# Kernel optimization log

Measured on AMD Instinct MI355X. Metric: run time of the kernel, lower is better.

## Reference

```python
import jax, jax.numpy as jnp
import numpy as np

B, T, E = 2, 2048, 1024
H = 16
D = E // H  # 64

def setup_inputs() -> dict:
    key = jax.random.key(0)
    kx, kq, kk, kv, ko = jax.random.split(key, 5)
    s = 1.0 / np.sqrt(E)
    return {
        "x":  jax.random.normal(kx, (B, T, E), dtype=jnp.float32),
        "Wq": jax.random.normal(kq, (E, E), dtype=jnp.float32) * s,
        "Wk": jax.random.normal(kk, (E, E), dtype=jnp.float32) * s,
        "Wv": jax.random.normal(kv, (E, E), dtype=jnp.float32) * s,
        "Wo": jax.random.normal(ko, (E, E), dtype=jnp.float32) * s,
    }

def reference(x, Wq, Wk, Wv, Wo):
    # Faithful to the torch module, including its quirks:
    #  - head split is a raw .view(B, H, T, D) reshape (NOT a transpose split)
    #  - masked_fill result is discarded in the original, so NO causal mask is applied
    #  - dropout = 0.0 -> identity
    b, t, e = x.shape
    q = jnp.reshape(x @ Wq, (b, H, t, D))
    k = jnp.reshape(x @ Wk, (b, H, t, D))
    v = jnp.reshape(x @ Wv, (b, H, t, D))
    # raw_score = q @ k^T ; softmax over keys of raw_score / sqrt(head_dim)
    scores = jnp.einsum("bhtd,bhsd->bhts", q, k) / jnp.sqrt(jnp.asarray(D, x.dtype))
    attn = jax.nn.softmax(scores, axis=-1)
    h = jnp.einsum("bhts,bhsd->bhtd", attn, v)           # (B,H,T,D)
    h = jnp.reshape(h, (b, t, e))                         # .view(B, T, -1)
    return h @ Wo
```

## Files before the change

### kernel.cpp

```cpp
#include <hip/hip_runtime.h>
#include <hip/hip_bf16.h>
#include <math.h>

#define BB 2
#define TT 2048
#define EE 1024
#define HH 16
#define DD 64
#define MM (BB*TT)

typedef __bf16 bf16;
typedef bf16 bf16x8 __attribute__((ext_vector_type(8)));
typedef bf16 bf16x4 __attribute__((ext_vector_type(4)));
typedef float f32x4 __attribute__((ext_vector_type(4)));

#define MFMA16(a,b,c) __builtin_amdgcn_mfma_f32_16x16x32_bf16((a),(b),(c),0,0,0)

__device__ __forceinline__ void gload_lds16(const void* g, void* l) {
  __builtin_amdgcn_global_load_lds(
      (const __attribute__((address_space(1))) unsigned int*)g,
      (__attribute__((address_space(3))) unsigned int*)l, 16, 0, 0);
}

__device__ __forceinline__ unsigned short bits(bf16 h) {
  return __builtin_bit_cast(unsigned short, h);
}

__global__ __launch_bounds__(256) void prep(const float* __restrict__ x,
                                            const float* __restrict__ w0,
                                            const float* __restrict__ w1,
                                            const float* __restrict__ w2,
                                            const float* __restrict__ w3,
                                            bf16* __restrict__ xb,
                                            bf16* t0, bf16* t1, bf16* t2, bf16* t3) {
  __shared__ bf16 tile[64][65];
  const int bid = blockIdx.x;
  if (bid < 4096) {
    const int i = bid * 256 + threadIdx.x;
    float4 f = ((const float4*)x)[i];
    bf16x4 h;
    h[0] = (bf16)f.x; h[1] = (bf16)f.y; h[2] = (bf16)f.z; h[3] = (bf16)f.w;
    ((bf16x4*)xb)[i] = h;
    return;
  }
  const int t = bid - 4096;
  const int z = t >> 8, rem = t & 255;
  const float* W = z == 0 ? w0 : z == 1 ? w1 : z == 2 ? w2 : w3;
  bf16* T = z == 0 ? t0 : z == 1 ? t1 : z == 2 ? t2 : t3;
  const int n0 = (rem & 15) * 64, k0 = (rem >> 4) * 64;
#pragma unroll
  for (int i = 0; i < 16; i++) {
    int idx = threadIdx.x + i * 256;
    int r = idx >> 6, c = idx & 63;
    tile[c][r] = (bf16)W[(size_t)(k0 + r) * EE + n0 + c];
  }
  __syncthreads();
#pragma unroll
  for (int i = 0; i < 16; i++) {
    int idx = threadIdx.x + i * 256;
    int r = idx >> 6, c = idx & 63;
    T[(size_t)(n0 + r) * EE + k0 + c] = tile[r][c];
  }
}

template <typename OutT>
__device__ __forceinline__ void gemm_core(const bf16* __restrict__ A, const bf16* __restrict__ Bt,
                                          OutT* __restrict__ C, bf16* As, bf16* Bs) {
  const int tid = threadIdx.x;
  const int w = tid >> 6, lane = tid & 63;
  const int lg = lane >> 4, lr = lane & 15;
  const int row0 = blockIdx.y * 128, col0 = blockIdx.x * 128;
  const int wrow = (w >> 1) * 64, wcol = (w & 1) * 64;
  f32x4 acc[4][4];
#pragma unroll
  for (int m = 0; m < 4; m++)
#pragma unroll
    for (int n = 0; n < 4; n++) acc[m][n] = f32x4{0.f, 0.f, 0.f, 0.f};

  for (int kt = 0; kt < EE; kt += 32) {
#pragma unroll
    for (int i = 0; i < 2; i++) {
      const int c = i * 4 + w;
      const int row = c * 16 + (lane >> 2);
      const int kof = (lane & 3) * 8;
      gload_lds16(A + (size_t)(row0 + row) * EE + kt + kof, &As[c * 512]);
      gload_lds16(Bt + (size_t)(col0 + row) * EE + kt + kof, &Bs[c * 512]);
    }
    __syncthreads();
    bf16x8 a[4], b[4];
#pragma unroll
    for (int m = 0; m < 4; m++)
      a[m] = *(const bf16x8*)&As[(wrow + m * 16 + lr) * 32 + lg * 8];
#pragma unroll
    for (int n = 0; n < 4; n++)
      b[n] = *(const bf16x8*)&Bs[(wcol + n * 16 + lr) * 32 + lg * 8];
#pragma unroll
    for (int m = 0; m < 4; m++)
#pragma unroll
      for (int n = 0; n < 4; n++) acc[m][n] = MFMA16(a[m], b[n], acc[m][n]);
    __syncthreads();
  }
#pragma unroll
  for (int m = 0; m < 4; m++)
#pragma unroll
    for (int n = 0; n < 4; n++)
#pragma unroll
      for (int r = 0; r < 4; r++) {
        const int rr = row0 + wrow + m * 16 + lg * 4 + r;
        const int cc = col0 + wcol + n * 16 + lr;
        C[(size_t)rr * EE + cc] = (OutT)acc[m][n][r];
      }
}

__global__ __launch_bounds__(256) void gemm_qkv(const bf16* __restrict__ A,
                                                const bf16* __restrict__ w0,
                                                const bf16* __restrict__ w1,
                                                const bf16* __restrict__ w2,
                                                bf16* o0, bf16* o1, bf16* o2) {
  __shared__ __align__(16) bf16 As[128 * 32];
  __shared__ __align__(16) bf16 Bs[128 * 32];
  const bf16* Bt = (blockIdx.z == 0) ? w0 : (blockIdx.z == 1) ? w1 : w2;
  bf16* C = (blockIdx.z == 0) ? o0 : (blockIdx.z == 1) ? o1 : o2;
  gemm_core<bf16>(A, Bt, C, As, Bs);
}

__global__ __launch_bounds__(256) void gemm_out(const bf16* __restrict__ A,
                                                const bf16* __restrict__ Bt,
                                                float* __restrict__ C) {
  __shared__ __align__(16) bf16 As[128 * 32];
  __shared__ __align__(16) bf16 Bs[128 * 32];
  gemm_core<float>(A, Bt, C, As, Bs);
}

__global__ __launch_bounds__(256, 2) void flash_attn(const bf16* __restrict__ Q,
                                                     const bf16* __restrict__ K,
                                                     const bf16* __restrict__ V,
                                                     bf16* __restrict__ Hout) {
  const int tid = threadIdx.x;
  const int w = tid >> 6, lane = tid & 63;
  const int hi = lane >> 4, lr = lane & 15;

  const int bid = blockIdx.x + 16 * blockIdx.y;
  const int sid = (bid & 7) * 64 + (bid >> 3);
  const int qb = sid & 15, bh = sid >> 4;

  const size_t base = (size_t)(bh >> 4) * TT * EE + (size_t)(bh & 15) * 128 * EE;
  const bf16* qh = Q + base;
  const bf16* kh = K + base;
  const bf16* vh = V + base;
  bf16* hh = Hout + base;
  const int r0w = qb * 128 + w * 32;

  __shared__ __align__(16) bf16 Ks[2][64 * 72];
  __shared__ __align__(16) bf16 Vt[2][64 * 72];
  __shared__ __align__(16) bf16 Ps[4 * 32 * 72];
  bf16* Pw = &Ps[w * 32 * 72];

  const float qscale = 0.18033688011112042f;
  bf16x8 aq[2][2];
#pragma unroll
  for (int rg = 0; rg < 2; rg++)
#pragma unroll
    for (int kk = 0; kk < 2; kk++) {
      bf16x8 qv = *(const bf16x8*)(qh + (size_t)(r0w + rg * 16 + lr) * DD + kk * 32 + hi * 8);
#pragma unroll
      for (int j = 0; j < 8; j++) qv[j] = (bf16)(qscale * (float)qv[j]);
      aq[rg][kk] = qv;
    }

  float l_[2] = {0.f, 0.f};
  f32x4 o[2][4];
#pragma unroll
  for (int rg = 0; rg < 2; rg++)
#pragma unroll
    for (int d = 0; d < 4; d++) o[rg][d] = f32x4{0.f, 0.f, 0.f, 0.f};

  const int krow = tid >> 2, kg8 = (tid & 3) * 8;
  const int vsp = tid & 31, vdb = (tid >> 5) * 4;

  bf16x8 kr0 = *(const bf16x8*)(kh + (size_t)krow * DD + kg8);
  bf16x8 kr1 = *(const bf16x8*)(kh + (size_t)krow * DD + kg8 + 32);
  bf16x4 va0 = *(const bf16x4*)(vh + (size_t)(2 * vsp) * DD + vdb);
  bf16x4 vb0 = *(const bf16x4*)(vh + (size_t)(2 * vsp + 1) * DD + vdb);
  bf16x4 va1 = *(const bf16x4*)(vh + (size_t)(2 * vsp) * DD + vdb + 32);
  bf16x4 vb1 = *(const bf16x4*)(vh + (size_t)(2 * vsp + 1) * DD + vdb + 32);
  *(bf16x8*)&Ks[0][krow * 72 + kg8] = kr0;
  *(bf16x8*)&Ks[0][krow * 72 + kg8 + 32] = kr1;
#pragma unroll
  for (int j = 0; j < 4; j++) {
    unsigned u0 = (unsigned)bits(va0[j]) | ((unsigned)bits(vb0[j]) << 16);
    unsigned u1 = (unsigned)bits(va1[j]) | ((unsigned)bits(vb1[j]) << 16);
    *(unsigned*)&Vt[0][(vdb + j) * 72 + 2 * vsp] = u0;
    *(unsigned*)&Vt[0][(vdb + 32 + j) * 72 + 2 * vsp] = u1;
  }
  kr0 = *(const bf16x8*)(kh + (size_t)(64 + krow) * DD + kg8);
  kr1 = *(const bf16x8*)(kh + (size_t)(64 + krow) * DD + kg8 + 32);
  va0 = *(const bf16x4*)(vh + (size_t)(64 + 2 * vsp) * DD + vdb);
  vb0 = *(const bf16x4*)(vh + (size_t)(64 + 2 * vsp + 1) * DD + vdb);
  va1 = *(const bf16x4*)(vh + (size_t)(64 + 2 * vsp) * DD + vdb + 32);
  vb1 = *(const bf16x4*)(vh + (size_t)(64 + 2 * vsp + 1) * DD + vdb + 32);
  __syncthreads();

  for (int t = 0; t < TT / 64; t++) {
    const bf16* Kc = Ks[t & 1];
    const bf16* Vc = Vt[t & 1];

    f32x4 sA[2][4];
#pragma unroll
    for (int rg = 0; rg < 2; rg++)
#pragma unroll
      for (int cf = 0; cf < 4; cf++) sA[rg][cf] = f32x4{0.f, 0.f, 0.f, 0.f};
#pragma unroll
    for (int cf = 0; cf < 4; cf++)
#pragma unroll
      for (int kk = 0; kk < 2; kk++) {
        bf16x8 bk = *(const bf16x8*)&Kc[(cf * 16 + lr) * 72 + kk * 32 + hi * 8];
#pragma unroll
        for (int rg = 0; rg < 2; rg++) sA[rg][cf] = MFMA16(bk, aq[rg][kk], sA[rg][cf]);
      }

#pragma unroll
    for (int rg = 0; rg < 2; rg++)
#pragma unroll
      for (int cf = 0; cf < 4; cf++) {
        bf16x4 pb;
#pragma unroll
        for (int r = 0; r < 4; r++) {
          float p = __builtin_amdgcn_exp2f(sA[rg][cf][r]);
          l_[rg] += p;
          pb[r] = (bf16)p;
        }
        *(bf16x4*)&Pw[(rg * 16 + lr) * 72 + cf * 16 + 4 * hi] = pb;
      }
    asm volatile("s_waitcnt lgkmcnt(0)" ::: "memory");

#pragma unroll
    for (int kk = 0; kk < 2; kk++) {
      bf16x8 bp[2];
#pragma unroll
      for (int rg = 0; rg < 2; rg++)
        bp[rg] = *(const bf16x8*)&Pw[(rg * 16 + lr) * 72 + kk * 32 + hi * 8];
#pragma unroll
      for (int dblk = 0; dblk < 4; dblk++) {
        bf16x8 av = *(const bf16x8*)&Vc[(dblk * 16 + lr) * 72 + kk * 32 + hi * 8];
#pragma unroll
        for (int rg = 0; rg < 2; rg++)
          o[rg][dblk] = MFMA16(av, bp[rg], o[rg][dblk]);
      }
    }

    if (t < TT / 64 - 1) {
      bf16* Kn = Ks[(t + 1) & 1];
      bf16* Vn = Vt[(t + 1) & 1];
      *(bf16x8*)&Kn[krow * 72 + kg8] = kr0;
      *(bf16x8*)&Kn[krow * 72 + kg8 + 32] = kr1;
#pragma unroll
      for (int j = 0; j < 4; j++) {
        unsigned u0 = (unsigned)bits(va0[j]) | ((unsigned)bits(vb0[j]) << 16);
        unsigned u1 = (unsigned)bits(va1[j]) | ((unsigned)bits(vb1[j]) << 16);
        *(unsigned*)&Vn[(vdb + j) * 72 + 2 * vsp] = u0;
        *(unsigned*)&Vn[(vdb + 32 + j) * 72 + 2 * vsp] = u1;
      }
      if (t < TT / 64 - 2) {
        const int s2 = (t + 2) * 64;
        kr0 = *(const bf16x8*)(kh + (size_t)(s2 + krow) * DD + kg8);
        kr1 = *(const bf16x8*)(kh + (size_t)(s2 + krow) * DD + kg8 + 32);
        va0 = *(const bf16x4*)(vh + (size_t)(s2 + 2 * vsp) * DD + vdb);
        vb0 = *(const bf16x4*)(vh + (size_t)(s2 + 2 * vsp + 1) * DD + vdb);
        va1 = *(const bf16x4*)(vh + (size_t)(s2 + 2 * vsp) * DD + vdb + 32);
        vb1 = *(const bf16x4*)(vh + (size_t)(s2 + 2 * vsp + 1) * DD + vdb + 32);
      }
    }
    __syncthreads();
  }

#pragma unroll
  for (int rg = 0; rg < 2; rg++) {
    float lt = l_[rg];
    lt += __shfl_xor(lt, 16);
    lt += __shfl_xor(lt, 32);
#pragma unroll
    for (int dblk = 0; dblk < 4; dblk++) {
      bf16x4 st;
#pragma unroll
      for (int r = 0; r < 4; r++) st[r] = (bf16)(o[rg][dblk][r] / lt);
      *(bf16x4*)(hh + (size_t)(r0w + rg * 16 + lr) * DD + dblk * 16 + 4 * hi) = st;
    }
  }
}

extern "C" void kernel_launch(void* const* d_in, const int* in_sizes, int n_in,
                              void* d_out, int out_size, void* d_ws, size_t ws_size,
                              hipStream_t stream) {
  const float* x  = (const float*)d_in[0];
  const float* Wq = (const float*)d_in[1];
  const float* Wk = (const float*)d_in[2];
  const float* Wv = (const float*)d_in[3];
  const float* Wo = (const float*)d_in[4];
  float* out = (float*)d_out;

  bf16* xb  = (bf16*)d_ws;
  bf16* wqt = xb + (size_t)MM * EE;
  bf16* wkt = wqt + (size_t)EE * EE;
  bf16* wvt = wkt + (size_t)EE * EE;
  bf16* wot = wvt + (size_t)EE * EE;
  bf16* Qb  = wot + (size_t)EE * EE;
  bf16* Kb  = Qb + (size_t)MM * EE;
  bf16* Vb  = Kb + (size_t)MM * EE;
  bf16* Hb  = xb;

  prep<<<dim3(5120), 256, 0, stream>>>(x, Wq, Wk, Wv, Wo, xb, wqt, wkt, wvt, wot);
  gemm_qkv<<<dim3(8, 32, 3), 256, 0, stream>>>(xb, wqt, wkt, wvt, Qb, Kb, Vb);
  flash_attn<<<dim3(16, 32), 256, 0, stream>>>(Qb, Kb, Vb, Hb);
  gemm_out<<<dim3(8, 32), 256, 0, stream>>>(Hb, wot, out);
}
```

Measured before the change: 122.3 us.

## Halve flash-attn query tile, load K fragments directly into registers

The attention kernel now gives each wave 16 query rows instead of 32, doubling the grid to 1024 blocks and raising the occupancy hint to 4 blocks per CU. K is no longer staged through LDS; each wave loads its MFMA K fragments straight from global memory into registers, prefetched one tile ahead. This cuts LDS traffic and footprint and improves parallelism. In exchange, K is reread from global/L2 by every wave, and reuse of each K/V tile across query rows is halved.

```diff
diff --git a/kernel.cpp b/kernel.cpp
--- a/kernel.cpp
+++ b/kernel.cpp
@@ -132,7 +132,7 @@
   gemm_core<float>(A, Bt, C, As, Bs);
 }
 
-__global__ __launch_bounds__(256, 2) void flash_attn(const bf16* __restrict__ Q,
+__global__ __launch_bounds__(256, 4) void flash_attn(const bf16* __restrict__ Q,
                                                      const bf16* __restrict__ K,
                                                      const bf16* __restrict__ V,
                                                      bf16* __restrict__ Hout) {
@@ -140,52 +140,49 @@
   const int w = tid >> 6, lane = tid & 63;
   const int hi = lane >> 4, lr = lane & 15;
 
-  const int bid = blockIdx.x + 16 * blockIdx.y;
-  const int sid = (bid & 7) * 64 + (bid >> 3);
-  const int qb = sid & 15, bh = sid >> 4;
+  const int bid = blockIdx.x + 32 * blockIdx.y;
+  const int sid = (bid & 7) * 128 + (bid >> 3);
+  const int qb = sid & 31, bh = sid >> 5;
 
   const size_t base = (size_t)(bh >> 4) * TT * EE + (size_t)(bh & 15) * 128 * EE;
   const bf16* qh = Q + base;
   const bf16* kh = K + base;
   const bf16* vh = V + base;
   bf16* hh = Hout + base;
-  const int r0w = qb * 128 + w * 32;
-
-  __shared__ __align__(16) bf16 Ks[2][64 * 72];
+  const int r0w = qb * 64 + w * 16;
+
   __shared__ __align__(16) bf16 Vt[2][64 * 72];
-  __shared__ __align__(16) bf16 Ps[4 * 32 * 72];
-  bf16* Pw = &Ps[w * 32 * 72];
+  __shared__ __align__(16) bf16 Ps[4 * 16 * 72];
+  bf16* Pw = &Ps[w * 16 * 72];
 
   const float qscale = 0.18033688011112042f;
-  bf16x8 aq[2][2];
-#pragma unroll
-  for (int rg = 0; rg < 2; rg++)
-#pragma unroll
-    for (int kk = 0; kk < 2; kk++) {
-      bf16x8 qv = *(const bf16x8*)(qh + (size_t)(r0w + rg * 16 + lr) * DD + kk * 32 + hi * 8);
-#pragma unroll
-      for (int j = 0; j < 8; j++) qv[j] = (bf16)(qscale * (float)qv[j]);
-      aq[rg][kk] = qv;
-    }
-
-  float l_[2] = {0.f, 0.f};
-  f32x4 o[2][4];
-#pragma unroll
-  for (int rg = 0; rg < 2; rg++)
-#pragma unroll
-    for (int d = 0; d < 4; d++) o[rg][d] = f32x4{0.f, 0.f, 0.f, 0.f};
-
-  const int krow = tid >> 2, kg8 = (tid & 3) * 8;
+  bf16x8 aq[2];
+#pragma unroll
+  for (int kk = 0; kk < 2; kk++) {
+    bf16x8 qv = *(const bf16x8*)(qh + (size_t)(r0w + lr) * DD + kk * 32 + hi * 8);
+#pragma unroll
+    for (int j = 0; j < 8; j++) qv[j] = (bf16)(qscale * (float)qv[j]);
+    aq[kk] = qv;
+  }
+
+  float l_ = 0.f;
+  f32x4 o[4];
+#pragma unroll
+  for (int d = 0; d < 4; d++) o[d] = f32x4{0.f, 0.f, 0.f, 0.f};
+
   const int vsp = tid & 31, vdb = (tid >> 5) * 4;
 
-  bf16x8 kr0 = *(const bf16x8*)(kh + (size_t)krow * DD + kg8);
-  bf16x8 kr1 = *(const bf16x8*)(kh + (size_t)krow * DD + kg8 + 32);
+  bf16x8 kf[4][2];
+#pragma unroll
+  for (int cf = 0; cf < 4; cf++)
+#pragma unroll
+    for (int kk = 0; kk < 2; kk++)
+      kf[cf][kk] = *(const bf16x8*)(kh + (size_t)(cf * 16 + lr) * DD + kk * 32 + hi * 8);
+
   bf16x4 va0 = *(const bf16x4*)(vh + (size_t)(2 * vsp) * DD + vdb);
   bf16x4 vb0 = *(const bf16x4*)(vh + (size_t)(2 * vsp + 1) * DD + vdb);
   bf16x4 va1 = *(const bf16x4*)(vh + (size_t)(2 * vsp) * DD + vdb + 32);
   bf16x4 vb1 = *(const bf16x4*)(vh + (size_t)(2 * vsp + 1) * DD + vdb + 32);
-  *(bf16x8*)&Ks[0][krow * 72 + kg8] = kr0;
-  *(bf16x8*)&Ks[0][krow * 72 + kg8 + 32] = kr1;
 #pragma unroll
   for (int j = 0; j < 4; j++) {
     unsigned u0 = (unsigned)bits(va0[j]) | ((unsigned)bits(vb0[j]) << 16);
@@ -193,8 +190,6 @@
     *(unsigned*)&Vt[0][(vdb + j) * 72 + 2 * vsp] = u0;
     *(unsigned*)&Vt[0][(vdb + 32 + j) * 72 + 2 * vsp] = u1;
   }
-  kr0 = *(const bf16x8*)(kh + (size_t)(64 + krow) * DD + kg8);
-  kr1 = *(const bf16x8*)(kh + (size_t)(64 + krow) * DD + kg8 + 32);
   va0 = *(const bf16x4*)(vh + (size_t)(64 + 2 * vsp) * DD + vdb);
   vb0 = *(const bf16x4*)(vh + (size_t)(64 + 2 * vsp + 1) * DD + vdb);
   va1 = *(const bf16x4*)(vh + (size_t)(64 + 2 * vsp) * DD + vdb + 32);
@@ -202,58 +197,50 @@
   __syncthreads();
 
   for (int t = 0; t < TT / 64; t++) {
-    const bf16* Kc = Ks[t & 1];
     const bf16* Vc = Vt[t & 1];
 
-    f32x4 sA[2][4];
-#pragma unroll
-    for (int rg = 0; rg < 2; rg++)
-#pragma unroll
-      for (int cf = 0; cf < 4; cf++) sA[rg][cf] = f32x4{0.f, 0.f, 0.f, 0.f};
+    f32x4 sA[4];
+#pragma unroll
+    for (int cf = 0; cf < 4; cf++) sA[cf] = f32x4{0.f, 0.f, 0.f, 0.f};
 #pragma unroll
     for (int cf = 0; cf < 4; cf++)
 #pragma unroll
-      for (int kk = 0; kk < 2; kk++) {
-        bf16x8 bk = *(const bf16x8*)&Kc[(cf * 16 + lr) * 72 + kk * 32 + hi * 8];
-#pragma unroll
-        for (int rg = 0; rg < 2; rg++) sA[rg][cf] = MFMA16(bk, aq[rg][kk], sA[rg][cf]);
-      }
-
-#pragma unroll
-    for (int rg = 0; rg < 2; rg++)
-#pragma unroll
-      for (int cf = 0; cf < 4; cf++) {
-        bf16x4 pb;
-#pragma unroll
-        for (int r = 0; r < 4; r++) {
-          float p = __builtin_amdgcn_exp2f(sA[rg][cf][r]);
-          l_[rg] += p;
-          pb[r] = (bf16)p;
-        }
-        *(bf16x4*)&Pw[(rg * 16 + lr) * 72 + cf * 16 + 4 * hi] = pb;
-      }
+      for (int kk = 0; kk < 2; kk++) sA[cf] = MFMA16(kf[cf][kk], aq[kk], sA[cf]);
+
+    if (t < TT / 64 - 1) {
+      const int s1 = (t + 1) * 64;
+#pragma unroll
+      for (int cf = 0; cf < 4; cf++)
+#pragma unroll
+        for (int kk = 0; kk < 2; kk++)
+          kf[cf][kk] = *(const bf16x8*)(kh + (size_t)(s1 + cf * 16 + lr) * DD + kk * 32 + hi * 8);
+    }
+
+#pragma unroll
+    for (int cf = 0; cf < 4; cf++) {
+      bf16x4 pb;
+#pragma unroll
+      for (int r = 0; r < 4; r++) {
+        float p = __builtin_amdgcn_exp2f(sA[cf][r]);
+        l_ += p;
+        pb[r] = (bf16)p;
+      }
+      *(bf16x4*)&Pw[lr * 72 + cf * 16 + 4 * hi] = pb;
+    }
     asm volatile("s_waitcnt lgkmcnt(0)" ::: "memory");
 
 #pragma unroll
     for (int kk = 0; kk < 2; kk++) {
-      bf16x8 bp[2];
-#pragma unroll
-      for (int rg = 0; rg < 2; rg++)
-        bp[rg] = *(const bf16x8*)&Pw[(rg * 16 + lr) * 72 + kk * 32 + hi * 8];
+      bf16x8 bp = *(const bf16x8*)&Pw[lr * 72 + kk * 32 + hi * 8];
 #pragma unroll
       for (int dblk = 0; dblk < 4; dblk++) {
         bf16x8 av = *(const bf16x8*)&Vc[(dblk * 16 + lr) * 72 + kk * 32 + hi * 8];
-#pragma unroll
-        for (int rg = 0; rg < 2; rg++)
-          o[rg][dblk] = MFMA16(av, bp[rg], o[rg][dblk]);
+        o[dblk] = MFMA16(av, bp, o[dblk]);
       }
     }
 
     if (t < TT / 64 - 1) {
-      bf16* Kn = Ks[(t + 1) & 1];
       bf16* Vn = Vt[(t + 1) & 1];
-      *(bf16x8*)&Kn[krow * 72 + kg8] = kr0;
-      *(bf16x8*)&Kn[krow * 72 + kg8 + 32] = kr1;
 #pragma unroll
       for (int j = 0; j < 4; j++) {
         unsigned u0 = (unsigned)bits(va0[j]) | ((unsigned)bits(vb0[j]) << 16);
@@ -263,8 +250,6 @@
       }
       if (t < TT / 64 - 2) {
         const int s2 = (t + 2) * 64;
-        kr0 = *(const bf16x8*)(kh + (size_t)(s2 + krow) * DD + kg8);
-        kr1 = *(const bf16x8*)(kh + (size_t)(s2 + krow) * DD + kg8 + 32);
         va0 = *(const bf16x4*)(vh + (size_t)(s2 + 2 * vsp) * DD + vdb);
         vb0 = *(const bf16x4*)(vh + (size_t)(s2 + 2 * vsp + 1) * DD + vdb);
         va1 = *(const bf16x4*)(vh + (size_t)(s2 + 2 * vsp) * DD + vdb + 32);
@@ -274,18 +259,15 @@
     __syncthreads();
   }
 
-#pragma unroll
-  for (int rg = 0; rg < 2; rg++) {
-    float lt = l_[rg];
-    lt += __shfl_xor(lt, 16);
-    lt += __shfl_xor(lt, 32);
-#pragma unroll
-    for (int dblk = 0; dblk < 4; dblk++) {
-      bf16x4 st;
-#pragma unroll
-      for (int r = 0; r < 4; r++) st[r] = (bf16)(o[rg][dblk][r] / lt);
-      *(bf16x4*)(hh + (size_t)(r0w + rg * 16 + lr) * DD + dblk * 16 + 4 * hi) = st;
-    }
+  float lt = l_;
+  lt += __shfl_xor(lt, 16);
+  lt += __shfl_xor(lt, 32);
+#pragma unroll
+  for (int dblk = 0; dblk < 4; dblk++) {
+    bf16x4 st;
+#pragma unroll
+    for (int r = 0; r < 4; r++) st[r] = (bf16)(o[dblk][r] / lt);
+    *(bf16x4*)(hh + (size_t)(r0w + lr) * DD + dblk * 16 + 4 * hi) = st;
   }
 }
 
@@ -311,6 +293,6 @@
 
   prep<<<dim3(5120), 256, 0, stream>>>(x, Wq, Wk, Wv, Wo, xb, wqt, wkt, wvt, wot);
   gemm_qkv<<<dim3(8, 32, 3), 256, 0, stream>>>(xb, wqt, wkt, wvt, Qb, Kb, Vb);
-  flash_attn<<<dim3(16, 32), 256, 0, stream>>>(Qb, Kb, Vb, Hb);
+  flash_attn<<<dim3(32, 32), 256, 0, stream>>>(Qb, Kb, Vb, Hb);
   gemm_out<<<dim3(8, 32), 256, 0, stream>>>(Hb, wot, out);
 }
```

New measurement: 240.8 us. +96.9%, slower.

## Keep softmax probabilities in registers by permuting V key columns in LDS

Applied to the files above, without the earlier changes.

Drops the per-warp LDS staging buffer for the probability tile. The P values now go straight from the QK^T MFMA accumulator registers into the B operand of the PV MFMA. To make this valid, the transposed V tile is written to shared memory with a permuted key-column order (vcs) that matches the accumulator's register layout. This removes an LDS write/read round trip, a wait, and LDS footprint, at the cost of a nonstandard V layout that must exactly match the MFMA fragment mapping.

```diff
diff --git a/kernel.cpp b/kernel.cpp
--- a/kernel.cpp
+++ b/kernel.cpp
@@ -153,8 +153,6 @@
 
   __shared__ __align__(16) bf16 Ks[2][64 * 72];
   __shared__ __align__(16) bf16 Vt[2][64 * 72];
-  __shared__ __align__(16) bf16 Ps[4 * 32 * 72];
-  bf16* Pw = &Ps[w * 32 * 72];
 
   const float qscale = 0.18033688011112042f;
   bf16x8 aq[2][2];
@@ -177,6 +175,8 @@
 
   const int krow = tid >> 2, kg8 = (tid & 3) * 8;
   const int vsp = tid & 31, vdb = (tid >> 5) * 4;
+  const int s0p = 2 * vsp;
+  const int vcs = (s0p & 32) | (((s0p >> 2) & 3) << 3) | (((s0p >> 4) & 1) << 2) | (s0p & 3);
 
   bf16x8 kr0 = *(const bf16x8*)(kh + (size_t)krow * DD + kg8);
   bf16x8 kr1 = *(const bf16x8*)(kh + (size_t)krow * DD + kg8 + 32);
@@ -190,8 +190,8 @@
   for (int j = 0; j < 4; j++) {
     unsigned u0 = (unsigned)bits(va0[j]) | ((unsigned)bits(vb0[j]) << 16);
     unsigned u1 = (unsigned)bits(va1[j]) | ((unsigned)bits(vb1[j]) << 16);
-    *(unsigned*)&Vt[0][(vdb + j) * 72 + 2 * vsp] = u0;
-    *(unsigned*)&Vt[0][(vdb + 32 + j) * 72 + 2 * vsp] = u1;
+    *(unsigned*)&Vt[0][(vdb + j) * 72 + vcs] = u0;
+    *(unsigned*)&Vt[0][(vdb + 32 + j) * 72 + vcs] = u1;
   }
   kr0 = *(const bf16x8*)(kh + (size_t)(64 + krow) * DD + kg8);
   kr1 = *(const bf16x8*)(kh + (size_t)(64 + krow) * DD + kg8 + 32);
@@ -219,35 +219,34 @@
         for (int rg = 0; rg < 2; rg++) sA[rg][cf] = MFMA16(bk, aq[rg][kk], sA[rg][cf]);
       }
 
-#pragma unroll
-    for (int rg = 0; rg < 2; rg++)
-#pragma unroll
-      for (int cf = 0; cf < 4; cf++) {
-        bf16x4 pb;
+    bf16x8 bp[2][2];
+#pragma unroll
+    for (int rg = 0; rg < 2; rg++) {
+      f32x4 pr[4];
+#pragma unroll
+      for (int cf = 0; cf < 4; cf++)
 #pragma unroll
         for (int r = 0; r < 4; r++) {
           float p = __builtin_amdgcn_exp2f(sA[rg][cf][r]);
           l_[rg] += p;
-          pb[r] = (bf16)p;
+          pr[cf][r] = p;
         }
-        *(bf16x4*)&Pw[(rg * 16 + lr) * 72 + cf * 16 + 4 * hi] = pb;
-      }
-    asm volatile("s_waitcnt lgkmcnt(0)" ::: "memory");
-
-#pragma unroll
-    for (int kk = 0; kk < 2; kk++) {
-      bf16x8 bp[2];
-#pragma unroll
-      for (int rg = 0; rg < 2; rg++)
-        bp[rg] = *(const bf16x8*)&Pw[(rg * 16 + lr) * 72 + kk * 32 + hi * 8];
+#pragma unroll
+      for (int kk = 0; kk < 2; kk++)
+#pragma unroll
+        for (int j = 0; j < 8; j++)
+          bp[rg][kk][j] = (bf16)pr[2 * kk + (j >> 2)][j & 3];
+    }
+
+#pragma unroll
+    for (int kk = 0; kk < 2; kk++)
 #pragma unroll
       for (int dblk = 0; dblk < 4; dblk++) {
         bf16x8 av = *(const bf16x8*)&Vc[(dblk * 16 + lr) * 72 + kk * 32 + hi * 8];
 #pragma unroll
         for (int rg = 0; rg < 2; rg++)
-          o[rg][dblk] = MFMA16(av, bp[rg], o[rg][dblk]);
-      }
-    }
+          o[rg][dblk] = MFMA16(av, bp[rg][kk], o[rg][dblk]);
+      }
 
     if (t < TT / 64 - 1) {
       bf16* Kn = Ks[(t + 1) & 1];
@@ -258,8 +257,8 @@
       for (int j = 0; j < 4; j++) {
         unsigned u0 = (unsigned)bits(va0[j]) | ((unsigned)bits(vb0[j]) << 16);
         unsigned u1 = (unsigned)bits(va1[j]) | ((unsigned)bits(vb1[j]) << 16);
-        *(unsigned*)&Vn[(vdb + j) * 72 + 2 * vsp] = u0;
-        *(unsigned*)&Vn[(vdb + 32 + j) * 72 + 2 * vsp] = u1;
+        *(unsigned*)&Vn[(vdb + j) * 72 + vcs] = u0;
+        *(unsigned*)&Vn[(vdb + 32 + j) * 72 + vcs] = u1;
       }
       if (t < TT / 64 - 2) {
         const int s2 = (t + 2) * 64;
```

After: 114.5 us. -6.4%, faster.
